# Kernel optimization log

Hardware: AMD Instinct MI355X
Metric: run time of the kernel (lower is better)

Reference implementation:

```python
import jax, jax.numpy as jnp
import numpy as np


def conv2d(x, w, b=None, pad=1):
    # x [B,C,H,W], w [O,I,kh,kw]
    out = jax.lax.conv_general_dilated(
        x, w, window_strides=(1, 1), padding=((pad, pad), (pad, pad)),
        dimension_numbers=("NCHW", "OIHW", "NCHW"))
    if b is not None:
        out = out + b[None, :, None, None]
    return out


def deform_conv(x, offset_w, offset_b, weight_w, pad=1):
    B, C, H, W = x.shape
    K2 = offset_w.shape[0] // 2  # k^2 sampling taps

    # offsets: [B, 2, K2, H, W]; channel 0 = x (width), 1 = y (height)
    offsets = conv2d(x, offset_w, offset_b, pad=pad).reshape(B, 2, K2, H, W)
    base = jnp.stack([
        jnp.broadcast_to(jnp.linspace(-1.0, 1.0, W)[None, :], (H, W)),
        jnp.broadcast_to(jnp.linspace(-1.0, 1.0, H)[:, None], (H, W)),
    ], axis=0)  # [2, H, W] in normalized [-1, 1] coords
    grid = offsets + base[None, :, None]  # [B, 2, K2, H, W]

    # grid_sample semantics: bilinear, zeros padding, align_corners=False
    gx = ((grid[:, 0] + 1.0) * W - 1.0) * 0.5  # [B, K2, H, W] pixel coords
    gy = ((grid[:, 1] + 1.0) * H - 1.0) * 0.5
    x0f = jnp.floor(gx); y0f = jnp.floor(gy)
    wx1 = gx - x0f; wx0 = 1.0 - wx1
    wy1 = gy - y0f; wy0 = 1.0 - wy1
    ix0 = x0f.astype(jnp.int32); ix1 = ix0 + 1
    iy0 = y0f.astype(jnp.int32); iy1 = iy0 + 1

    x_flat = x.reshape(B, C, H * W)

    def gather(ix, iy):
        valid = (ix >= 0) & (ix < W) & (iy >= 0) & (iy < H)  # [B,K2,H,W]
        idx = (jnp.clip(iy, 0, H - 1) * W + jnp.clip(ix, 0, W - 1)).reshape(B, 1, -1)
        v = jnp.take_along_axis(x_flat, idx, axis=2).reshape(B, C, K2, H, W)
        return v * valid[:, None].astype(x.dtype)

    sampled = (gather(ix0, iy0) * (wx0 * wy0)[:, None]
               + gather(ix1, iy0) * (wx1 * wy0)[:, None]
               + gather(ix0, iy1) * (wx0 * wy1)[:, None]
               + gather(ix1, iy1) * (wx1 * wy1)[:, None])  # [B,C,K2,H,W]

    # weighted sum over taps with per-(channel, tap) weights from weight_conv
    wk = weight_w.reshape(C, K2)
    return jnp.einsum('bckhw,ck->bchw', sampled, wk)


def setup_inputs() -> dict:
    key = jax.random.key(0)
    B, C, S, k = 8, 128, 64, 3
    k0, k1, k2 = jax.random.split(key, 3)
    x = jax.random.normal(k0, (B, C, S, S), dtype=jnp.float32)
    # original zero-inits the offset conv; small random weights exercise the gathers
    offset_w = jax.random.normal(k1, (2 * k * k, C, k, k), dtype=jnp.float32) * 0.01
    offset_b = jnp.zeros((2 * k * k,), dtype=jnp.float32)
    weight_w = jax.random.normal(k2, (1, C, k, k), dtype=jnp.float32) * 0.05
    return {"x": x, "offset_w": offset_w, "offset_b": offset_b, "weight_w": weight_w}


def reference(x, offset_w, offset_b, weight_w):
    return deform_conv(x, offset_w, offset_b, weight_w, pad=1)
```

## Files before the change

kernel.cpp:

```cpp
#include <hip/hip_runtime.h>

#define BB 8
#define CC 128
#define HH 64
#define WW 64
#define K2 9
#define NOFF 18
#define HW 4096
#define NPIX 32768
#define OPAD 32
#define HP 66
#define PSTRIDE (HP*HP*CC)

#define TR_BLOCKS     4096
#define WF_BLOCKS     288
#define BORDER_BLOCKS 260
#define SAMPLE_BLOCKS 2048

#define GR_ROW 1056
#define ROWSET_BYTES 33792

typedef __attribute__((ext_vector_type(8))) short bf16x8;
typedef __attribute__((ext_vector_type(4))) float f32x4;

__device__ __forceinline__ unsigned short f2bf(float f) {
    unsigned u = __float_as_uint(f);
    unsigned r = u + 0x7FFFu + ((u >> 16) & 1u);
    return (unsigned short)(r >> 16);
}
__device__ __forceinline__ float bf2f(unsigned short h) {
    return __uint_as_float((unsigned)h << 16);
}

__global__ __launch_bounds__(256) void prep_transpose_kernel(
    const float* __restrict__ x, const float* __restrict__ offw,
    unsigned short* __restrict__ xPh, unsigned short* __restrict__ xPl,
    unsigned short* __restrict__ wF)
{
    __shared__ float tile[32][33];
    int bi = blockIdx.x;
    int tid = threadIdx.x;
    if (bi < TR_BLOCKS) {
        int p0 = (bi & 127) * 32;
        int c0 = ((bi >> 7) & 3) * 32;
        int b  = bi >> 9;
        int tx = tid & 31;
        int ty = tid >> 5;
#pragma unroll
        for (int i = 0; i < 4; ++i)
            tile[ty + i * 8][tx] =
                x[((size_t)(b * CC + c0 + ty + i * 8)) * HW + p0 + tx];
        __syncthreads();
#pragma unroll
        for (int i = 0; i < 4; ++i) {
            int p = p0 + ty + i * 8;
            int h = p >> 6, w = p & 63;
            float v = tile[tx][ty + i * 8];
            unsigned short hi = f2bf(v);
            unsigned short lo = f2bf(v - bf2f(hi));
            size_t pidx = ((size_t)b * HP * HP + (size_t)(h + 1) * HP + (w + 1)) * CC + c0 + tx;
            xPh[pidx] = hi;
            xPl[pidx] = lo;
        }
    } else if (bi < TR_BLOCKS + WF_BLOCKS) {
        int e = (bi - TR_BLOCKS) * 256 + tid;
        int fid = e >> 9;
        int r = e & 511;
        int lane = r >> 3;
        int elem = r & 7;
        int bufsel = fid & 1;
        int n   = (fid >> 1) & 1;
        int cwv = (fid >> 2) & 3;
        int j   = fid >> 4;
        int o = n * 16 + (lane & 15);
        int c = cwv * 32 + ((lane >> 4) << 3) + elem;
        float v = (o < NOFF) ? offw[((size_t)o * CC + c) * K2 + j] : 0.f;
        unsigned short hi = f2bf(v);
        wF[e] = bufsel ? f2bf(v - bf2f(hi)) : hi;
    } else {
        int i = (bi - TR_BLOCKS - WF_BLOCKS) * 256 + tid;
        int bufsel = i >= 33280;
        int jj = i - bufsel * 33280;
        int cell = jj >> 4, q = jj & 15;
        int b = cell / 260, r = cell - b * 260;
        int hp, wp;
        if (r < 132) { hp = (r >= 66) ? (HP - 1) : 0; wp = (r >= 66) ? r - 66 : r; }
        else { int r2 = r - 132; wp = (r2 & 1) ? (HP - 1) : 0; hp = 1 + (r2 >> 1); }
        unsigned short* dst = bufsel ? xPl : xPh;
        uint4 z = {0u, 0u, 0u, 0u};
        *(uint4*)(dst + (((size_t)b * HP + hp) * HP + wp) * CC + q * 8) = z;
    }
}

__global__ __launch_bounds__(256, 2) void offset_mfma_kernel(
    const unsigned short* __restrict__ xPh, const unsigned short* __restrict__ xPl,
    const unsigned short* __restrict__ wF,
    const float* __restrict__ offb, float2* __restrict__ sgrid)
{
    __shared__ __align__(16) unsigned char LDSB[ROWSET_BYTES];
    int jx = blockIdx.x;
    int b = jx & 7;
    int h = jx >> 3;
    int tid = threadIdx.x;
    int l = tid & 63;
    int cw = __builtin_amdgcn_readfirstlane(tid >> 6);
    int row  = l & 15;
    int kseg = l >> 4;
    int cslot = cw * 4 + kseg;

    f32x4 acc[4][2];
#pragma unroll
    for (int m = 0; m < 4; ++m)
#pragma unroll
        for (int n = 0; n < 2; ++n)
            acc[m][n] = (f32x4){0.f, 0.f, 0.f, 0.f};

    const unsigned short* xh = xPh + (size_t)b * PSTRIDE;
    const unsigned short* xl = xPl + (size_t)b * PSTRIDE;

#pragma unroll 1
    for (int dh = 0; dh < 3; ++dh) {
        if (dh) __syncthreads();
        const unsigned short* rowh = xh + ((size_t)(h + dh) * HP) * CC;
        const unsigned short* rowl = xl + ((size_t)(h + dh) * HP) * CC;
#pragma unroll
        for (int it = 0; it < 9; ++it) {
            int G = it * 256 + tid;
            if (G < 2112) {
                int buf = G >= GR_ROW;
                int g = G - (buf ? GR_ROW : 0);
                int px = g >> 4, cg = g & 15;
                const unsigned short* src =
                    (buf ? rowl : rowh) + (size_t)px * CC + ((cg ^ (px & 7)) << 3);
                uint4 v = *(const uint4*)src;
                *(uint4*)(LDSB + (size_t)G * 16) = v;
            }
        }
        __syncthreads();
#pragma unroll
        for (int dw = 0; dw < 3; ++dw) {
            int j = dh * 3 + dw;
            int fbase = (j * 4 + cw) * 4;
            bf16x8 Bh0 = *(const bf16x8*)(wF + (size_t)(fbase + 0) * 512 + l * 8);
            bf16x8 Bl0 = *(const bf16x8*)(wF + (size_t)(fbase + 1) * 512 + l * 8);
            bf16x8 Bh1 = *(const bf16x8*)(wF + (size_t)(fbase + 2) * 512 + l * 8);
            bf16x8 Bl1 = *(const bf16x8*)(wF + (size_t)(fbase + 3) * 512 + l * 8);
#pragma unroll
            for (int m = 0; m < 4; ++m) {
                int px = m * 16 + row + dw;
                int gA = px * 16 + (cslot ^ (px & 7));
                bf16x8 Ah = *(const bf16x8*)(LDSB + (size_t)gA * 16);
                bf16x8 Al = *(const bf16x8*)(LDSB + (size_t)(GR_ROW + gA) * 16);
                acc[m][0] = __builtin_amdgcn_mfma_f32_16x16x32_bf16(Ah, Bh0, acc[m][0], 0, 0, 0);
                acc[m][0] = __builtin_amdgcn_mfma_f32_16x16x32_bf16(Al, Bh0, acc[m][0], 0, 0, 0);
                acc[m][0] = __builtin_amdgcn_mfma_f32_16x16x32_bf16(Ah, Bl0, acc[m][0], 0, 0, 0);
                acc[m][1] = __builtin_amdgcn_mfma_f32_16x16x32_bf16(Ah, Bh1, acc[m][1], 0, 0, 0);
                acc[m][1] = __builtin_amdgcn_mfma_f32_16x16x32_bf16(Al, Bh1, acc[m][1], 0, 0, 0);
                acc[m][1] = __builtin_amdgcn_mfma_f32_16x16x32_bf16(Ah, Bl1, acc[m][1], 0, 0, 0);
            }
        }
    }

    __syncthreads();
    float (*red)[OPAD][65] = (float (*)[OPAD][65])LDSB;
#pragma unroll
    for (int m = 0; m < 4; ++m)
#pragma unroll
        for (int n = 0; n < 2; ++n)
#pragma unroll
            for (int r = 0; r < 4; ++r)
                red[cw][n * 16 + row][m * 16 + kseg * 4 + r] = acc[m][n][r];
    __syncthreads();

    for (int item = tid; item < 576; item += 256) {
        int p = item & 63;
        int t = item >> 6;
        float sx = offb[t]
                 + red[0][t][p] + red[1][t][p] + red[2][t][p] + red[3][t][p];
        float sy = offb[t + K2]
                 + red[0][t + K2][p] + red[1][t + K2][p]
                 + red[2][t + K2][p] + red[3][t + K2][p];
        float base_x = -1.f + (2.f / (WW - 1)) * (float)p;
        float base_y = -1.f + (2.f / (HH - 1)) * (float)h;
        float gx = ((sx + base_x + 1.f) * (float)WW - 1.f) * 0.5f;
        float gy = ((sy + base_y + 1.f) * (float)HH - 1.f) * 0.5f;
        sgrid[(size_t)t * NPIX + b * HW + h * WW + p] = make_float2(gx, gy);
    }
}

__global__ __launch_bounds__(256, 4) void sample_kernel(
    const unsigned short* __restrict__ xPh, const float2* __restrict__ sgrid,
    const float* __restrict__ wk, float* __restrict__ out)
{
    __shared__ float4 recW[144];
    __shared__ int2   recI[144];
    __shared__ float  swkT[K2 * CC];
    __shared__ float  acc_s[16 * 132];

    int j = blockIdx.x;
    int b = j & 7;
    int rem_base = (j >> 3) * 16;
    int h  = rem_base >> 6;
    int w0 = rem_base & 63;
    int tid = threadIdx.x;

    for (int i = tid; i < K2 * CC; i += 256) {
        int c = i / 9, t = i - c * 9;
        swkT[t * CC + c] = wk[i];
    }

    if (tid < 144) {
        int slot = tid & 15;
        int tap  = tid >> 4;
        int rem  = rem_base + slot;
        int pix  = b * HW + rem;
        float2 s = sgrid[(size_t)tap * NPIX + pix];
        float gx = s.x, gy = s.y;

        float x0f = floorf(gx), y0f = floorf(gy);
        float wx1 = gx - x0f, wx0 = 1.f - wx1;
        float wy1 = gy - y0f, wy0 = 1.f - wy1;
        int ix0 = (int)x0f, iy0 = (int)y0f;
        int ix1 = ix0 + 1,  iy1 = iy0 + 1;
        float ax0 = ((unsigned)ix0 < WW) ? wx0 : 0.f;
        float ax1 = ((unsigned)ix1 < WW) ? wx1 : 0.f;
        float ay0 = ((unsigned)iy0 < HH) ? wy0 : 0.f;
        float ay1 = ((unsigned)iy1 < HH) ? wy1 : 0.f;
        int cx0 = min(max(ix0, 0), WW - 1) + 1, cx1 = min(max(ix1, 0), WW - 1) + 1;
        int cy0 = min(max(iy0, 0), HH - 1) + 1, cy1 = min(max(iy1, 0), HH - 1) + 1;
        int o00 = cy0 * HP + cx0, o10 = cy0 * HP + cx1;
        int o01 = cy1 * HP + cx0, o11 = cy1 * HP + cx1;
        recW[tid] = make_float4(ax0 * ay0, ax1 * ay0, ax0 * ay1, ax1 * ay1);
        recI[tid] = make_int2(o00 | (o10 << 16), o01 | (o11 << 16));
    }
    __syncthreads();

    int c8   = (tid & 15) * 8;
    int slot = tid >> 4;

    const unsigned short* xb = xPh + (size_t)b * PSTRIDE;

    float acc[8];
#pragma unroll
    for (int i = 0; i < 8; ++i) acc[i] = 0.f;

#pragma unroll
    for (int t = 0; t < K2; ++t) {
        int r = t * 16 + slot;
        float4 wv = recW[r];
        int2   iv = recI[r];
        uint4 u00 = *(const uint4*)(xb + (((iv.x & 0xFFFF) << 7) + c8));
        uint4 u10 = *(const uint4*)(xb + (((iv.x >> 16)     << 7) + c8));
        uint4 u01 = *(const uint4*)(xb + (((iv.y & 0xFFFF) << 7) + c8));
        uint4 u11 = *(const uint4*)(xb + (((iv.y >> 16)     << 7) + c8));
        float4 wkA = *(const float4*)&swkT[t * CC + c8];
        float4 wkB = *(const float4*)&swkT[t * CC + c8 + 4];
        const unsigned* p00 = (const unsigned*)&u00;
        const unsigned* p10 = (const unsigned*)&u10;
        const unsigned* p01 = (const unsigned*)&u01;
        const unsigned* p11 = (const unsigned*)&u11;
#pragma unroll
        for (int g = 0; g < 4; ++g) {
            float v00a = __uint_as_float(p00[g] << 16);
            float v00b = __uint_as_float(p00[g] & 0xFFFF0000u);
            float v10a = __uint_as_float(p10[g] << 16);
            float v10b = __uint_as_float(p10[g] & 0xFFFF0000u);
            float v01a = __uint_as_float(p01[g] << 16);
            float v01b = __uint_as_float(p01[g] & 0xFFFF0000u);
            float v11a = __uint_as_float(p11[g] << 16);
            float v11b = __uint_as_float(p11[g] & 0xFFFF0000u);
            float bila = fmaf(v00a, wv.x, fmaf(v10a, wv.y, fmaf(v01a, wv.z, v11a * wv.w)));
            float bilb = fmaf(v00b, wv.x, fmaf(v10b, wv.y, fmaf(v01b, wv.z, v11b * wv.w)));
            float wka = (g < 2) ? ((g == 0) ? wkA.x : wkA.z)
                                : ((g == 2) ? wkB.x : wkB.z);
            float wkb = (g < 2) ? ((g == 0) ? wkA.y : wkA.w)
                                : ((g == 2) ? wkB.y : wkB.w);
            acc[g * 2]     = fmaf(bila, wka, acc[g * 2]);
            acc[g * 2 + 1] = fmaf(bilb, wkb, acc[g * 2 + 1]);
        }
    }

    *(float4*)&acc_s[slot * 132 + c8]     = make_float4(acc[0], acc[1], acc[2], acc[3]);
    *(float4*)&acc_s[slot * 132 + c8 + 4] = make_float4(acc[4], acc[5], acc[6], acc[7]);
    __syncthreads();
#pragma unroll
    for (int r = 0; r < 8; ++r) {
        int cs   = r * 16 + (tid >> 4);
        int wloc = tid & 15;
        out[((size_t)(b * CC + cs)) * HW + h * WW + w0 + wloc] = acc_s[wloc * 132 + cs];
    }
}

__global__ __launch_bounds__(256) void offset_grid_kernel_fb(
    const float* __restrict__ x, const float* __restrict__ offw,
    const float* __restrict__ offb, float* __restrict__ grid)
{
    int idx = blockIdx.x * blockDim.x + threadIdx.x;
    if (idx >= NPIX) return;
    int w = idx & 63, h = (idx >> 6) & 63, b = idx >> 12;
    float acc[NOFF];
#pragma unroll
    for (int o = 0; o < NOFF; ++o) acc[o] = offb[o];
    for (int c = 0; c < CC; ++c) {
        const float* xp = x + ((size_t)(b * CC + c)) * HW;
        float xv[9];
#pragma unroll
        for (int dh = -1; dh <= 1; ++dh)
#pragma unroll
            for (int dw = -1; dw <= 1; ++dw) {
                int hh = h + dh, ww2 = w + dw;
                float v = 0.f;
                if (hh >= 0 && hh < HH && ww2 >= 0 && ww2 < WW) v = xp[hh * WW + ww2];
                xv[(dh + 1) * 3 + (dw + 1)] = v;
            }
#pragma unroll
        for (int o = 0; o < NOFF; ++o) {
            const float* wp = offw + (size_t)(o * CC + c) * 9;
#pragma unroll
            for (int jj = 0; jj < 9; ++jj) acc[o] = fmaf(xv[jj], wp[jj], acc[o]);
        }
    }
    float base_x = -1.f + (2.f / (WW - 1)) * (float)w;
    float base_y = -1.f + (2.f / (HH - 1)) * (float)h;
#pragma unroll
    for (int t = 0; t < K2; ++t) {
        float gx = ((acc[t]      + base_x + 1.f) * (float)WW - 1.f) * 0.5f;
        float gy = ((acc[K2 + t] + base_y + 1.f) * (float)HH - 1.f) * 0.5f;
        size_t gi = ((((size_t)b * K2 + t) * HH + h) * WW + w) * 2;
        grid[gi] = gx; grid[gi + 1] = gy;
    }
}

__global__ __launch_bounds__(256) void sample_kernel_fb(
    const float* __restrict__ x, const float* __restrict__ grid,
    const float* __restrict__ wk, float* __restrict__ out)
{
    int idx = blockIdx.x * blockDim.x + threadIdx.x;
    if (idx >= BB * CC * HW) return;
    int w = idx & 63, h = (idx >> 6) & 63;
    int c = (idx / HW) & 127, b = idx / (CC * HW);
    const float* xp = x + ((size_t)(b * CC + c)) * HW;
    const float2* gp = (const float2*)grid;
    float acc = 0.f;
#pragma unroll
    for (int t = 0; t < K2; ++t) {
        float2 g = gp[(((size_t)b * K2 + t)) * HW + h * WW + w];
        float gx = g.x, gy = g.y;
        float x0f = floorf(gx), y0f = floorf(gy);
        float wx1 = gx - x0f, wx0 = 1.f - wx1;
        float wy1 = gy - y0f, wy0 = 1.f - wy1;
        int ix0 = (int)x0f, iy0 = (int)y0f;
        int ix1 = ix0 + 1,  iy1 = iy0 + 1;
        float v00 = 0.f, v10 = 0.f, v01 = 0.f, v11 = 0.f;
        if ((unsigned)iy0 < HH) {
            const float* row = xp + (size_t)iy0 * WW;
            if ((unsigned)ix0 < WW) v00 = row[ix0];
            if ((unsigned)ix1 < WW) v10 = row[ix1];
        }
        if ((unsigned)iy1 < HH) {
            const float* row = xp + (size_t)iy1 * WW;
            if ((unsigned)ix0 < WW) v01 = row[ix0];
            if ((unsigned)ix1 < WW) v11 = row[ix1];
        }
        float bil = v00 * (wx0 * wy0) + v10 * (wx1 * wy0)
                  + v01 * (wx0 * wy1) + v11 * (wx1 * wy1);
        acc = fmaf(bil, wk[c * K2 + t], acc);
    }
    out[idx] = acc;
}

extern "C" void kernel_launch(void* const* d_in, const int* in_sizes, int n_in,
                              void* d_out, int out_size, void* d_ws, size_t ws_size,
                              hipStream_t stream) {
    const float* x    = (const float*)d_in[0];
    const float* offw = (const float*)d_in[1];
    const float* offb = (const float*)d_in[2];
    const float* wwk  = (const float*)d_in[3];
    float* out = (float*)d_out;

    const size_t SGRID_BYTES = (size_t)K2 * NPIX * sizeof(float2);
    const size_t XP_BYTES    = (size_t)BB * PSTRIDE * sizeof(unsigned short);
    const size_t WF_BYTES    = (size_t)144 * 512 * sizeof(unsigned short);
    const size_t NEED = SGRID_BYTES + 2 * XP_BYTES + WF_BYTES;

    if (ws_size < NEED) {
        float* grid = (float*)d_ws;
        hipLaunchKernelGGL(offset_grid_kernel_fb, dim3(NPIX / 256), dim3(256),
                           0, stream, x, offw, offb, grid);
        hipLaunchKernelGGL(sample_kernel_fb, dim3((BB * CC * HW) / 256), dim3(256),
                           0, stream, x, grid, wwk, out);
        return;
    }

    char* p = (char*)d_ws;
    float2*         sgrid = (float2*)p;                 p += SGRID_BYTES;
    unsigned short* xPh = (unsigned short*)p;           p += XP_BYTES;
    unsigned short* xPl = (unsigned short*)p;           p += XP_BYTES;
    unsigned short* wF  = (unsigned short*)p;

    hipLaunchKernelGGL(prep_transpose_kernel,
                       dim3(TR_BLOCKS + WF_BLOCKS + BORDER_BLOCKS), dim3(256),
                       0, stream, x, offw, xPh, xPl, wF);
    hipLaunchKernelGGL(offset_mfma_kernel, dim3(512), dim3(256),
                       0, stream, xPh, xPl, wF, offb, sgrid);
    hipLaunchKernelGGL(sample_kernel, dim3(SAMPLE_BLOCKS), dim3(256),
                       0, stream, xPh, sgrid, wwk, out);
}
```

Before: 45.62 us.

## Fuse offset-conv MFMA kernel with bilinear sampling kernel

Merges the offset convolution kernel and the sampling kernel into a single kernel. Each block computes the sampling grid for one image row in shared memory and then immediately gathers and reduces over all 64 pixels of that row. This drops the sgrid round trip through global memory and one kernel launch. In exchange the sampling work now runs on only 512 blocks at occupancy 2 instead of 2048 blocks at occupancy 4, and shared memory use per block grows, which reduces latency hiding for the gathers.

```diff
diff --git a/kernel.cpp b/kernel.cpp
--- a/kernel.cpp
+++ b/kernel.cpp
@@ -15,7 +15,6 @@
 #define TR_BLOCKS     4096
 #define WF_BLOCKS     288
 #define BORDER_BLOCKS 260
-#define SAMPLE_BLOCKS 2048
 
 #define GR_ROW 1056
 #define ROWSET_BYTES 33792
@@ -92,12 +91,15 @@
     }
 }
 
-__global__ __launch_bounds__(256, 2) void offset_mfma_kernel(
+__global__ __launch_bounds__(256, 2) void fused_conv_sample_kernel(
     const unsigned short* __restrict__ xPh, const unsigned short* __restrict__ xPl,
-    const unsigned short* __restrict__ wF,
-    const float* __restrict__ offb, float2* __restrict__ sgrid)
+    const unsigned short* __restrict__ wF, const float* __restrict__ offb,
+    const float* __restrict__ wk, float* __restrict__ out)
 {
     __shared__ __align__(16) unsigned char LDSB[ROWSET_BYTES];
+    __shared__ float4 recW[576];
+    __shared__ int2   recI[576];
+    __shared__ float  swkT[K2 * CC];
     int jx = blockIdx.x;
     int b = jx & 7;
     int h = jx >> 3;
@@ -107,6 +109,11 @@
     int row  = l & 15;
     int kseg = l >> 4;
     int cslot = cw * 4 + kseg;
+
+    for (int i = tid; i < K2 * CC; i += 256) {
+        int c = i / 9, t = i - c * 9;
+        swkT[t * CC + c] = wk[i];
+    }
 
     f32x4 acc[4][2];
 #pragma unroll
@@ -172,6 +179,7 @@
                 red[cw][n * 16 + row][m * 16 + kseg * 4 + r] = acc[m][n][r];
     __syncthreads();
 
+    float base_y = -1.f + (2.f / (HH - 1)) * (float)h;
     for (int item = tid; item < 576; item += 256) {
         int p = item & 63;
         int t = item >> 6;
@@ -181,41 +189,8 @@
                  + red[0][t + K2][p] + red[1][t + K2][p]
                  + red[2][t + K2][p] + red[3][t + K2][p];
         float base_x = -1.f + (2.f / (WW - 1)) * (float)p;
-        float base_y = -1.f + (2.f / (HH - 1)) * (float)h;
         float gx = ((sx + base_x + 1.f) * (float)WW - 1.f) * 0.5f;
         float gy = ((sy + base_y + 1.f) * (float)HH - 1.f) * 0.5f;
-        sgrid[(size_t)t * NPIX + b * HW + h * WW + p] = make_float2(gx, gy);
-    }
-}
-
-__global__ __launch_bounds__(256, 4) void sample_kernel(
-    const unsigned short* __restrict__ xPh, const float2* __restrict__ sgrid,
-    const float* __restrict__ wk, float* __restrict__ out)
-{
-    __shared__ float4 recW[144];
-    __shared__ int2   recI[144];
-    __shared__ float  swkT[K2 * CC];
-    __shared__ float  acc_s[16 * 132];
-
-    int j = blockIdx.x;
-    int b = j & 7;
-    int rem_base = (j >> 3) * 16;
-    int h  = rem_base >> 6;
-    int w0 = rem_base & 63;
-    int tid = threadIdx.x;
-
-    for (int i = tid; i < K2 * CC; i += 256) {
-        int c = i / 9, t = i - c * 9;
-        swkT[t * CC + c] = wk[i];
-    }
-
-    if (tid < 144) {
-        int slot = tid & 15;
-        int tap  = tid >> 4;
-        int rem  = rem_base + slot;
-        int pix  = b * HW + rem;
-        float2 s = sgrid[(size_t)tap * NPIX + pix];
-        float gx = s.x, gy = s.y;
 
         float x0f = floorf(gx), y0f = floorf(gy);
         float wx1 = gx - x0f, wx0 = 1.f - wx1;
@@ -230,64 +205,73 @@
         int cy0 = min(max(iy0, 0), HH - 1) + 1, cy1 = min(max(iy1, 0), HH - 1) + 1;
         int o00 = cy0 * HP + cx0, o10 = cy0 * HP + cx1;
         int o01 = cy1 * HP + cx0, o11 = cy1 * HP + cx1;
-        recW[tid] = make_float4(ax0 * ay0, ax1 * ay0, ax0 * ay1, ax1 * ay1);
-        recI[tid] = make_int2(o00 | (o10 << 16), o01 | (o11 << 16));
+        recW[t * 64 + p] = make_float4(ax0 * ay0, ax1 * ay0, ax0 * ay1, ax1 * ay1);
+        recI[t * 64 + p] = make_int2(o00 | (o10 << 16), o01 | (o11 << 16));
     }
     __syncthreads();
 
-    int c8   = (tid & 15) * 8;
-    int slot = tid >> 4;
-
-    const unsigned short* xb = xPh + (size_t)b * PSTRIDE;
-
-    float acc[8];
-#pragma unroll
-    for (int i = 0; i < 8; ++i) acc[i] = 0.f;
-
+    int c8     = (tid & 15) * 8;
+    int slot16 = tid >> 4;
+    const unsigned short* xb = xh;
+    float* acc_s = (float*)LDSB;
+
+    float4 wkA[K2], wkB[K2];
 #pragma unroll
     for (int t = 0; t < K2; ++t) {
-        int r = t * 16 + slot;
-        float4 wv = recW[r];
-        int2   iv = recI[r];
-        uint4 u00 = *(const uint4*)(xb + (((iv.x & 0xFFFF) << 7) + c8));
-        uint4 u10 = *(const uint4*)(xb + (((iv.x >> 16)     << 7) + c8));
-        uint4 u01 = *(const uint4*)(xb + (((iv.y & 0xFFFF) << 7) + c8));
-        uint4 u11 = *(const uint4*)(xb + (((iv.y >> 16)     << 7) + c8));
-        float4 wkA = *(const float4*)&swkT[t * CC + c8];
-        float4 wkB = *(const float4*)&swkT[t * CC + c8 + 4];
-        const unsigned* p00 = (const unsigned*)&u00;
-        const unsigned* p10 = (const unsigned*)&u10;
-        const unsigned* p01 = (const unsigned*)&u01;
-        const unsigned* p11 = (const unsigned*)&u11;
-#pragma unroll
-        for (int g = 0; g < 4; ++g) {
-            float v00a = __uint_as_float(p00[g] << 16);
-            float v00b = __uint_as_float(p00[g] & 0xFFFF0000u);
-            float v10a = __uint_as_float(p10[g] << 16);
-            float v10b = __uint_as_float(p10[g] & 0xFFFF0000u);
-            float v01a = __uint_as_float(p01[g] << 16);
-            float v01b = __uint_as_float(p01[g] & 0xFFFF0000u);
-            float v11a = __uint_as_float(p11[g] << 16);
-            float v11b = __uint_as_float(p11[g] & 0xFFFF0000u);
-            float bila = fmaf(v00a, wv.x, fmaf(v10a, wv.y, fmaf(v01a, wv.z, v11a * wv.w)));
-            float bilb = fmaf(v00b, wv.x, fmaf(v10b, wv.y, fmaf(v01b, wv.z, v11b * wv.w)));
-            float wka = (g < 2) ? ((g == 0) ? wkA.x : wkA.z)
-                                : ((g == 2) ? wkB.x : wkB.z);
-            float wkb = (g < 2) ? ((g == 0) ? wkA.y : wkA.w)
-                                : ((g == 2) ? wkB.y : wkB.w);
-            acc[g * 2]     = fmaf(bila, wka, acc[g * 2]);
-            acc[g * 2 + 1] = fmaf(bilb, wkb, acc[g * 2 + 1]);
-        }
-    }
-
-    *(float4*)&acc_s[slot * 132 + c8]     = make_float4(acc[0], acc[1], acc[2], acc[3]);
-    *(float4*)&acc_s[slot * 132 + c8 + 4] = make_float4(acc[4], acc[5], acc[6], acc[7]);
-    __syncthreads();
-#pragma unroll
-    for (int r = 0; r < 8; ++r) {
-        int cs   = r * 16 + (tid >> 4);
-        int wloc = tid & 15;
-        out[((size_t)(b * CC + cs)) * HW + h * WW + w0 + wloc] = acc_s[wloc * 132 + cs];
+        wkA[t] = *(const float4*)&swkT[t * CC + c8];
+        wkB[t] = *(const float4*)&swkT[t * CC + c8 + 4];
+    }
+
+#pragma unroll 1
+    for (int pp = 0; pp < 4; ++pp) {
+        int slot = pp * 16 + slot16;
+        float acc8[8];
+#pragma unroll
+        for (int i = 0; i < 8; ++i) acc8[i] = 0.f;
+#pragma unroll
+        for (int t = 0; t < K2; ++t) {
+            int r = t * 64 + slot;
+            float4 wv = recW[r];
+            int2   iv = recI[r];
+            uint4 u00 = *(const uint4*)(xb + (((iv.x & 0xFFFF) << 7) + c8));
+            uint4 u10 = *(const uint4*)(xb + (((iv.x >> 16)     << 7) + c8));
+            uint4 u01 = *(const uint4*)(xb + (((iv.y & 0xFFFF) << 7) + c8));
+            uint4 u11 = *(const uint4*)(xb + (((iv.y >> 16)     << 7) + c8));
+            const unsigned* p00 = (const unsigned*)&u00;
+            const unsigned* p10 = (const unsigned*)&u10;
+            const unsigned* p01 = (const unsigned*)&u01;
+            const unsigned* p11 = (const unsigned*)&u11;
+#pragma unroll
+            for (int g = 0; g < 4; ++g) {
+                float v00a = __uint_as_float(p00[g] << 16);
+                float v00b = __uint_as_float(p00[g] & 0xFFFF0000u);
+                float v10a = __uint_as_float(p10[g] << 16);
+                float v10b = __uint_as_float(p10[g] & 0xFFFF0000u);
+                float v01a = __uint_as_float(p01[g] << 16);
+                float v01b = __uint_as_float(p01[g] & 0xFFFF0000u);
+                float v11a = __uint_as_float(p11[g] << 16);
+                float v11b = __uint_as_float(p11[g] & 0xFFFF0000u);
+                float bila = fmaf(v00a, wv.x, fmaf(v10a, wv.y, fmaf(v01a, wv.z, v11a * wv.w)));
+                float bilb = fmaf(v00b, wv.x, fmaf(v10b, wv.y, fmaf(v01b, wv.z, v11b * wv.w)));
+                float wka = (g < 2) ? ((g == 0) ? wkA[t].x : wkA[t].z)
+                                    : ((g == 2) ? wkB[t].x : wkB[t].z);
+                float wkb = (g < 2) ? ((g == 0) ? wkA[t].y : wkA[t].w)
+                                    : ((g == 2) ? wkB[t].y : wkB[t].w);
+                acc8[g * 2]     = fmaf(bila, wka, acc8[g * 2]);
+                acc8[g * 2 + 1] = fmaf(bilb, wkb, acc8[g * 2 + 1]);
+            }
+        }
+        __syncthreads();
+        *(float4*)&acc_s[slot16 * 132 + c8]     = make_float4(acc8[0], acc8[1], acc8[2], acc8[3]);
+        *(float4*)&acc_s[slot16 * 132 + c8 + 4] = make_float4(acc8[4], acc8[5], acc8[6], acc8[7]);
+        __syncthreads();
+#pragma unroll
+        for (int r = 0; r < 8; ++r) {
+            int cs   = r * 16 + (tid >> 4);
+            int wloc = tid & 15;
+            out[((size_t)(b * CC + cs)) * HW + h * WW + pp * 16 + wloc] =
+                acc_s[wloc * 132 + cs];
+        }
     }
 }
 
@@ -378,10 +362,9 @@
     const float* wwk  = (const float*)d_in[3];
     float* out = (float*)d_out;
 
-    const size_t SGRID_BYTES = (size_t)K2 * NPIX * sizeof(float2);
-    const size_t XP_BYTES    = (size_t)BB * PSTRIDE * sizeof(unsigned short);
-    const size_t WF_BYTES    = (size_t)144 * 512 * sizeof(unsigned short);
-    const size_t NEED = SGRID_BYTES + 2 * XP_BYTES + WF_BYTES;
+    const size_t XP_BYTES = (size_t)BB * PSTRIDE * sizeof(unsigned short);
+    const size_t WF_BYTES = (size_t)144 * 512 * sizeof(unsigned short);
+    const size_t NEED = 2 * XP_BYTES + WF_BYTES;
 
     if (ws_size < NEED) {
         float* grid = (float*)d_ws;
@@ -393,7 +376,6 @@
     }
 
     char* p = (char*)d_ws;
-    float2*         sgrid = (float2*)p;                 p += SGRID_BYTES;
     unsigned short* xPh = (unsigned short*)p;           p += XP_BYTES;
     unsigned short* xPl = (unsigned short*)p;           p += XP_BYTES;
     unsigned short* wF  = (unsigned short*)p;
@@ -401,8 +383,6 @@
     hipLaunchKernelGGL(prep_transpose_kernel,
                        dim3(TR_BLOCKS + WF_BLOCKS + BORDER_BLOCKS), dim3(256),
                        0, stream, x, offw, xPh, xPl, wF);
-    hipLaunchKernelGGL(offset_mfma_kernel, dim3(512), dim3(256),
-                       0, stream, xPh, xPl, wF, offb, sgrid);
-    hipLaunchKernelGGL(sample_kernel, dim3(SAMPLE_BLOCKS), dim3(256),
-                       0, stream, xPh, sgrid, wwk, out);
-}
+    hipLaunchKernelGGL(fused_conv_sample_kernel, dim3(512), dim3(256),
+                       0, stream, xPh, xPl, wF, offb, wwk, out);
+}
```

After: 44.55 us (median of 3 runs). 1.02x faster.
